# Kernel optimization log

Measured on AMD Instinct MI355X. Metric: run time of the kernel, lower is better.

Reference implementation:

```python
import jax, jax.numpy as jnp
import numpy as np

TOP_K = 3
TEMP = 5.0
EPS = 1e-12

def _normalize(x):
    # F.normalize(dim=-1): x / max(||x||_2, eps)
    n = jnp.linalg.norm(x, axis=-1, keepdims=True)
    return x / jnp.maximum(n, EPS)

def setup_inputs() -> dict:
    key = jax.random.key(0)
    ks = jax.random.split(key, 6)
    B, D, P = 32768, 512, 4096
    return {
        "regime_vector": jax.random.normal(ks[0], (B, D), dtype=jnp.float32),
        "prototypes": jax.random.normal(ks[1], (P, D), dtype=jnp.float32) * 0.1,
        "W1": jax.random.normal(ks[2], (32, 2 * D), dtype=jnp.float32) * 0.02,
        "b1": jax.random.normal(ks[3], (32,), dtype=jnp.float32) * 0.01,
        "W2": jax.random.normal(ks[4], (16, 32), dtype=jnp.float32) * 0.1,
        "b2": jax.random.normal(ks[5], (16,), dtype=jnp.float32) * 0.01,
    }

def reference(regime_vector, prototypes, W1, b1, W2, b2):
    # Cosine similarities: [B, P]
    sims = _normalize(regime_vector) @ _normalize(prototypes).T
    top_sims, top_idx = jax.lax.top_k(sims, TOP_K)          # [B, K]
    weights = jax.nn.softmax(top_sims * TEMP, axis=-1)       # [B, K]
    # Gather candidate prototypes: [B, K, D]
    cand = prototypes[top_idx]
    # Concat(regime, pattern) along feature dim: [B, K, 2D]
    B, K, D = cand.shape
    combined = jnp.concatenate(
        [jnp.broadcast_to(regime_vector[:, None, :], (B, K, D)), cand], axis=-1)
    # Two-layer MLP (torch Linear: x @ W.T + b)
    h = jax.nn.relu(jnp.einsum('bkd,hd->bkh', combined, W1) + b1)  # [B, K, 32]
    feats = jnp.einsum('bkh,oh->bko', h, W2) + b2                  # [B, K, 16]
    # Softmax-weighted sum over the K candidates
    pattern_features = jnp.einsum('bk,bko->bo', weights, feats)    # [B, 16]
    return pattern_features
```

## Files before the change

kernel.cpp:

```cpp
#include <hip/hip_runtime.h>
#include <stdint.h>


#define BDIM 512
#define NB   32768
#define NP   4096
#define PCH  256

typedef float  f32x4 __attribute__((ext_vector_type(4)));
typedef short  s16x8 __attribute__((ext_vector_type(8)));
typedef unsigned short u16;

typedef const __attribute__((address_space(1))) unsigned int* gas_t;
typedef __attribute__((address_space(3))) unsigned int* las_t;

__device__ __forceinline__ void gll16(const void* g, void* l) {
  __builtin_amdgcn_global_load_lds((gas_t)g, (las_t)l, 16, 0, 0);
}

__device__ __forceinline__ u16 f2bf(float f) {
  uint32_t u = __float_as_uint(f);
  return (u16)((u + 0x7FFFu + ((u >> 16) & 1u)) >> 16);
}
__device__ __forceinline__ uint32_t umx(uint32_t a, uint32_t b) { return a > b ? a : b; }
__device__ __forceinline__ uint32_t umn(uint32_t a, uint32_t b) { return a > b ? b : a; }

__device__ __forceinline__ uint32_t packkey(float v, int col) {
  uint32_t u = __float_as_uint(v);
  uint32_t mp = u ^ (uint32_t)(((int)u >> 31) | 0x80000000);
  return (mp & 0xFFFFF000u) | (uint32_t)col;
}
__device__ __forceinline__ float unpackf(uint32_t k) {
  uint32_t mbits = k & 0xFFFFF000u;
  uint32_t u = (mbits & 0x80000000u) ? (mbits ^ 0x80000000u) : ~mbits;
  return __uint_as_float(u);
}

__device__ __forceinline__ void bmerge(uint32_t* a, const uint32_t* b) {
  uint32_t t[8];
#pragma unroll
  for (int i = 0; i < 8; ++i) t[i] = umx(a[i], b[7 - i]);
#pragma unroll
  for (int i = 0; i < 4; ++i) { uint32_t x = umx(t[i], t[i + 4]), y = umn(t[i], t[i + 4]); t[i] = x; t[i + 4] = y; }
#pragma unroll
  for (int g = 0; g < 8; g += 4)
#pragma unroll
    for (int i = 0; i < 2; ++i) { uint32_t x = umx(t[g + i], t[g + i + 2]), y = umn(t[g + i], t[g + i + 2]); t[g + i] = x; t[g + i + 2] = y; }
#pragma unroll
  for (int p = 0; p < 8; p += 2) { uint32_t x = umx(t[p], t[p + 1]), y = umn(t[p], t[p + 1]); t[p] = x; t[p + 1] = y; }
#pragma unroll
  for (int i = 0; i < 8; ++i) a[i] = t[i];
}
__device__ __forceinline__ void mergeshfl(uint32_t* a, int mask) {
  uint32_t b[8];
#pragma unroll
  for (int i = 0; i < 8; ++i) b[i] = (uint32_t)__shfl_xor((int)a[i], mask, 64);
  bmerge(a, b);
}

__global__ __launch_bounds__(256) void prep_kernel(
    const float* __restrict__ src, const float* __restrict__ W1, int w1_off,
    int mode, u16* __restrict__ obf, float* __restrict__ onrm,
    float* __restrict__ oproj, float* __restrict__ onf32)
{
  __shared__ float rows[16][512];
  __shared__ float pscr[16][8][32];
  const int t = threadIdx.x, l = t & 63, w = t >> 6;
  const long rowbase = (long)blockIdx.x * 16;

  {
    const int r = t >> 4, c0 = (t & 15) * 32;
    const float4* gp = (const float4*)(src + (rowbase + r) * BDIM + c0);
    float4* dp = (float4*)&rows[r][c0];
#pragma unroll
    for (int i = 0; i < 8; ++i) dp[i] = gp[i];
  }
  float wreg[64];
  {
    const int h = t & 31, seg = t >> 5;
    const float* wp = W1 + h * 1024 + w1_off + seg * 64;
#pragma unroll
    for (int i = 0; i < 64; ++i) wreg[i] = wp[i];
  }
  __syncthreads();

#pragma unroll
  for (int i = 0; i < 4; ++i) {
    const int r = w * 4 + i;
    const long row = rowbase + r;
    float4 a = *(const float4*)&rows[r][4 * l];
    float4 c = *(const float4*)&rows[r][256 + 4 * l];
    float ss = a.x * a.x + a.y * a.y + a.z * a.z + a.w * a.w
             + c.x * c.x + c.y * c.y + c.z * c.z + c.w * c.w;
#pragma unroll
    for (int msk = 1; msk < 64; msk <<= 1) ss += __shfl_xor(ss, msk, 64);
    const float n = fmaxf(sqrtf(ss), 1e-12f);
    float4 qa, qc;
    qa.x = a.x / n; qa.y = a.y / n; qa.z = a.z / n; qa.w = a.w / n;
    qc.x = c.x / n; qc.y = c.y / n; qc.z = c.z / n; qc.w = c.w / n;
    ushort4 u0, u1;
    u0.x = f2bf(qa.x); u0.y = f2bf(qa.y); u0.z = f2bf(qa.z); u0.w = f2bf(qa.w);
    u1.x = f2bf(qc.x); u1.y = f2bf(qc.y); u1.z = f2bf(qc.z); u1.w = f2bf(qc.w);
    if (mode == 0) {
      if (l == 0) onrm[row] = n;
      *(ushort4*)(obf + row * BDIM + 4 * l) = u0;
      *(ushort4*)(obf + row * BDIM + 256 + 4 * l) = u1;
    } else {
      char* base = (char*)obf;
      *(ushort4*)(base + ((long)(l >> 4) * NP + row) * 128 + 8 * (l & 15)) = u0;
      *(ushort4*)(base + ((long)(4 + (l >> 4)) * NP + row) * 128 + 8 * (l & 15)) = u1;
      *(float4*)(onf32 + row * BDIM + 4 * l) = qa;
      *(float4*)(onf32 + row * BDIM + 256 + 4 * l) = qc;
    }
  }

  const int h = t & 31, seg = t >> 5;
  for (int r = 0; r < 16; ++r) {
    float p = 0.f;
#pragma unroll
    for (int j = 0; j < 16; ++j) {
      const float4 rv = *(const float4*)&rows[r][seg * 64 + 4 * j];
      p = fmaf(wreg[4 * j + 0], rv.x, p);
      p = fmaf(wreg[4 * j + 1], rv.y, p);
      p = fmaf(wreg[4 * j + 2], rv.z, p);
      p = fmaf(wreg[4 * j + 3], rv.w, p);
    }
    pscr[r][seg][h] = p;
  }
  __syncthreads();
#pragma unroll
  for (int q = 0; q < 2; ++q) {
    const int idx = t + q * 256;
    const int rr = idx >> 5, hh = idx & 31;
    float s = 0.f;
#pragma unroll
    for (int sg = 0; sg < 8; ++sg) s += pscr[rr][sg][hh];
    oproj[(rowbase + rr) * 32 + hh] = s;
  }
}

__global__ __launch_bounds__(256, 2) void topk_kernel(
    const u16* __restrict__ Rn,
    const u16* __restrict__ Pk,
    uint32_t* __restrict__ keys8)
{
  __shared__ uint4 lds4[5120];
  char* ldsb = (char*)lds4;

  const int t = threadIdx.x, l = t & 63, wid = t >> 6;
  const int wp = wid >> 1;
  const int wr = wid & 1;
  const int g = l >> 4, m = l & 15;
  const long rb = (long)blockIdx.x * 64;
  const char* Pkb = (const char*)Pk;
  const char* Rnb = (const char*)Rn;
  const int swsrc = 16 * ((l & 7) ^ ((l >> 3) & 7));
  const int lrow8 = (l >> 3);

  f32x4 acc[8][2];
  uint32_t k3[2][3];
  float thr[2];
#pragma unroll
  for (int fn = 0; fn < 2; ++fn) {
    thr[fn] = -1e30f;
#pragma unroll
    for (int i = 0; i < 3; ++i) k3[fn][i] = 0u;
  }

#define ISSUE(buf, ni_, kp_)                                                   \
  do {                                                                         \
    char* lp_ = ldsb + (buf) * 40960;                                          \
    const char* pg = Pkb + ((long)(kp_) * NP + (ni_) * PCH) * 128;             \
    _Pragma("unroll")                                                          \
    for (int i_ = 0; i_ < 8; ++i_) {                                           \
      const int ch_ = wid * 8 + i_;                                            \
      gll16(pg + ch_ * 1024 + lrow8 * 128 + swsrc, lp_ + ch_ * 1024);          \
    }                                                                          \
    _Pragma("unroll")                                                          \
    for (int j_ = 0; j_ < 2; ++j_) {                                           \
      const int ch_ = wid * 2 + j_;                                            \
      gll16(Rnb + (rb + ch_ * 8 + lrow8) * 1024 + (kp_) * 128 + swsrc,         \
            lp_ + 32768 + ch_ * 1024);                                         \
    }                                                                          \
  } while (0)

  ISSUE(0, 0, 0);

  for (int ni = 0; ni < 16; ++ni) {
#pragma unroll
    for (int fm = 0; fm < 8; ++fm)
#pragma unroll
      for (int fn = 0; fn < 2; ++fn) acc[fm][fn] = (f32x4){0.f, 0.f, 0.f, 0.f};

    for (int kp = 0; kp < 8; ++kp) {
      const int ph = ni * 8 + kp;
      asm volatile("s_waitcnt vmcnt(0)" ::: "memory");
      __builtin_amdgcn_s_barrier();
      const int nph = ph + 1;
      if (nph < 128) ISSUE(nph & 1, nph >> 3, nph & 7);
      __builtin_amdgcn_sched_barrier(0);
      const char* lp = ldsb + (ph & 1) * 40960;
      const char* lr = lp + 32768;
      const int sw = 16 * (m & 7);
#pragma unroll
      for (int ks = 0; ks < 2; ++ks) {
        const int koff = (ks * 64 + 16 * g) ^ sw;
        const char* pbr = lr + (wr * 32 + m) * 128 + koff;
        const char* pa = lp + (wp * 128 + m) * 128 + koff;
        uint4 b0 = *(const uint4*)(pbr);
        uint4 b1 = *(const uint4*)(pbr + 2048);
#pragma unroll
        for (int fm = 0; fm < 8; ++fm) {
          uint4 a4 = *(const uint4*)(pa + fm * 2048);
          acc[fm][0] = __builtin_amdgcn_mfma_f32_16x16x32_bf16(
              __builtin_bit_cast(s16x8, a4), __builtin_bit_cast(s16x8, b0),
              acc[fm][0], 0, 0, 0);
          acc[fm][1] = __builtin_amdgcn_mfma_f32_16x16x32_bf16(
              __builtin_bit_cast(s16x8, a4), __builtin_bit_cast(s16x8, b1),
              acc[fm][1], 0, 0, 0);
        }
      }
    }

    const int pb0 = ni * PCH + wp * 128 + 4 * g;
#pragma unroll
    for (int fn = 0; fn < 2; ++fn) {
#pragma unroll
      for (int fm = 0; fm < 8; ++fm) {
        const f32x4 v = acc[fm][fn];
        const float m4 = fmaxf(fmaxf(v[0], v[1]), fmaxf(v[2], v[3]));
        if (m4 > thr[fn]) {
#pragma unroll
          for (int r = 0; r < 4; ++r) {
            uint32_t kk = packkey(v[r], pb0 + fm * 16 + r);
            uint32_t mx0 = umx(k3[fn][0], kk), mn0 = umn(k3[fn][0], kk);
            k3[fn][0] = mx0; kk = mn0;
            uint32_t mx1 = umx(k3[fn][1], kk), mn1 = umn(k3[fn][1], kk);
            k3[fn][1] = mx1; kk = mn1;
            k3[fn][2] = umx(k3[fn][2], kk);
          }
          thr[fn] = unpackf(k3[fn][2]);
        }
      }
    }
  }
#undef ISSUE

  uint32_t* mrg = (uint32_t*)ldsb;
  uint32_t cur[2][8];
#pragma unroll
  for (int fn = 0; fn < 2; ++fn) {
    cur[fn][0] = k3[fn][0]; cur[fn][1] = k3[fn][1]; cur[fn][2] = k3[fn][2];
#pragma unroll
    for (int i = 3; i < 8; ++i) cur[fn][i] = 0u;
    mergeshfl(cur[fn], 16);
    mergeshfl(cur[fn], 32);
  }
  __syncthreads();
#pragma unroll
  for (int fn = 0; fn < 2; ++fn)
    if (wp == 1 && g == fn) {
      uint32_t* d = mrg + (wr * 32 + fn * 16 + m) * 8;
      uint4 a; a.x = cur[fn][0]; a.y = cur[fn][1]; a.z = cur[fn][2]; a.w = cur[fn][3];
      uint4 b; b.x = cur[fn][4]; b.y = cur[fn][5]; b.z = cur[fn][6]; b.w = cur[fn][7];
      *(uint4*)(d) = a; *(uint4*)(d + 4) = b;
    }
  __syncthreads();
#pragma unroll
  for (int fn = 0; fn < 2; ++fn)
    if (wp == 0 && g == fn) {
      const int row = wr * 32 + fn * 16 + m;
      uint32_t oth[8];
#pragma unroll
      for (int i = 0; i < 8; ++i) oth[i] = mrg[row * 8 + i];
      bmerge(cur[fn], oth);
      uint32_t* d = keys8 + (rb + row) * 8;
      uint4 a; a.x = cur[fn][0]; a.y = cur[fn][1]; a.z = cur[fn][2]; a.w = cur[fn][3];
      uint4 b; b.x = cur[fn][4]; b.y = cur[fn][5]; b.z = cur[fn][6]; b.w = cur[fn][7];
      *(uint4*)(d) = a; *(uint4*)(d + 4) = b;
    }
}

__global__ __launch_bounds__(256) void finalize_kernel(
    const float* __restrict__ regime, const float* __restrict__ protoNf,
    const uint32_t* __restrict__ keys8, const float* __restrict__ nrm_r,
    const float* __restrict__ rproj, const float* __restrict__ cproj,
    const float* __restrict__ b1, const float* __restrict__ W2,
    const float* __restrict__ b2, float* __restrict__ out)
{
  __shared__ float rlds[4][512];
  const int t = threadIdx.x, l = t & 63, w = t >> 6;
  const long b = (long)blockIdx.x * 4 + w;

  {
    const float n = nrm_r[b];
    const float4* gp = (const float4*)(regime + b * BDIM);
    float4 v0 = gp[l], v1 = gp[64 + l];
    v0.x /= n; v0.y /= n; v0.z /= n; v0.w /= n;
    v1.x /= n; v1.y /= n; v1.z /= n; v1.w /= n;
    *(float4*)&rlds[w][4 * l] = v0;
    *(float4*)&rlds[w][256 + 4 * l] = v1;
  }
  __syncthreads();

  const int j = l >> 3;
  const uint32_t key = keys8[b * 8 + j];
  const int pj = (int)(key & 0xFFFu);

  double dd = 0.0;
  {
    const float4* pp = (const float4*)(protoNf + (long)pj * BDIM);
    const float4* rr = (const float4*)&rlds[w][0];
#pragma unroll
    for (int u = 0; u < 16; ++u) {
      const float4 p4 = pp[(l & 7) + 8 * u];
      const float4 r4 = rr[(l & 7) + 8 * u];
      dd = fma((double)p4.x, (double)r4.x, dd);
      dd = fma((double)p4.y, (double)r4.y, dd);
      dd = fma((double)p4.z, (double)r4.z, dd);
      dd = fma((double)p4.w, (double)r4.w, dd);
    }
  }
  dd += __shfl_xor(dd, 1, 64);
  dd += __shfl_xor(dd, 2, 64);
  dd += __shfl_xor(dd, 4, 64);

  double sall[8]; int pall[8];
#pragma unroll
  for (int q = 0; q < 8; ++q) {
    sall[q] = __shfl(dd, q * 8, 64);
    pall[q] = __shfl(pj, q * 8, 64);
  }
  double vv[3]; int ppi[3]; unsigned chosen = 0;
#pragma unroll
  for (int r = 0; r < 3; ++r) {
    double bv = -1e301; int bp = 0x7FFFFFFF; int bq = 0;
#pragma unroll
    for (int q = 0; q < 8; ++q) {
      const bool ex = (chosen >> q) & 1u;
      const bool better = !ex && ((sall[q] > bv) || (sall[q] == bv && pall[q] < bp));
      bv = better ? sall[q] : bv;
      bp = better ? pall[q] : bp;
      bq = better ? q : bq;
    }
    vv[r] = bv; ppi[r] = bp; chosen |= 1u << bq;
  }
  const float v0f = (float)vv[0], v1f = (float)vv[1], v2f = (float)vv[2];
  const float e1 = expf(5.f * (v1f - v0f));
  const float e2 = expf(5.f * (v2f - v0f));
  const float winv = 1.f / (1.f + e1 + e2);
  const float w0 = winv, w1 = e1 * winv, w2 = e2 * winv;

  const int hu = l & 31, o = l & 15;
  const float rpv = rproj[b * 32 + hu];
  const float b1v = b1[hu];
  float w2row[32];
#pragma unroll
  for (int hh = 0; hh < 32; ++hh) w2row[hh] = W2[o * 32 + hh];
  float outacc = (l < 16) ? b2[o] : 0.f;
#pragma unroll
  for (int k = 0; k < 3; ++k) {
    const float cpv = cproj[(long)ppi[k] * 32 + hu];
    const float hval = fmaxf(rpv + cpv + b1v, 0.f);
    float f = 0.f;
#pragma unroll
    for (int hh = 0; hh < 32; ++hh) f = fmaf(w2row[hh], __shfl(hval, hh, 64), f);
    const float wk = (k == 0) ? w0 : ((k == 1) ? w1 : w2);
    outacc = fmaf(wk, f, outacc);
  }
  if (l < 16) out[b * 16 + o] = outacc;
}

extern "C" void kernel_launch(void* const* d_in, const int* in_sizes, int n_in,
                              void* d_out, int out_size, void* d_ws, size_t ws_size,
                              hipStream_t stream)
{
  (void)in_sizes; (void)n_in; (void)out_size; (void)ws_size;
  const float* regime = (const float*)d_in[0];
  const float* protos = (const float*)d_in[1];
  const float* W1     = (const float*)d_in[2];
  const float* b1     = (const float*)d_in[3];
  const float* W2     = (const float*)d_in[4];
  const float* b2     = (const float*)d_in[5];
  float* out = (float*)d_out;

  char* ws = (char*)d_ws;
  u16*      protoK  = (u16*)ws;      ws += (size_t)NP * BDIM * 2;
  u16*      regimeN = (u16*)ws;      ws += (size_t)NB * BDIM * 2;
  float*    protoNf = (float*)ws;    ws += (size_t)NP * BDIM * 4;
  float*    nrm_r   = (float*)ws;    ws += (size_t)NB * 4;
  float*    cproj   = (float*)ws;    ws += (size_t)NP * 32 * 4;
  float*    rproj   = (float*)ws;    ws += (size_t)NB * 32 * 4;
  uint32_t* keys8   = (uint32_t*)ws; ws += (size_t)NB * 8 * 4;

  hipLaunchKernelGGL(prep_kernel, dim3(NP / 16), dim3(256), 0, stream,
                     protos, W1, 512, 1, protoK, (float*)nullptr, cproj, protoNf);
  hipLaunchKernelGGL(prep_kernel, dim3(NB / 16), dim3(256), 0, stream,
                     regime, W1, 0, 0, regimeN, nrm_r, rproj, (float*)nullptr);
  hipLaunchKernelGGL(topk_kernel, dim3(512), dim3(256), 0, stream,
                     regimeN, protoK, keys8);
  hipLaunchKernelGGL(finalize_kernel, dim3(NB / 4), dim3(256), 0, stream,
                     regime, protoNf, keys8, nrm_r, rproj, cproj, b1, W2, b2, out);
}
```

Measured before the change: 425.6 us.

## Restructure top-k GEMM: 32x32 MFMA, register-streamed prototypes, LDS-resident regime rows

The similarity kernel is rebuilt. Each 512-thread block now loads 128 normalized regime rows into LDS once. Prototype fragments stream straight from global memory into registers with double buffering, replacing the per-phase LDS staging and barriers, and the 16x16x32 MFMA is swapped for 32x32x16. The prep kernel writes prototypes in a new fragment-ready layout to match. The cross-wave merge becomes an LDS gather followed by insertion into a top-8. Finalize now skips the fp64 rescoring dot product for candidates that clearly cannot reach the top 3. The cost is more registers per thread and a heavier load on global and L2 bandwidth for prototype reads. The approximate-score cutoff in finalize could change tie handling if the 4e-3 margin is too tight.

Result: slower. 573.4 us (+34.7%).

```diff
diff --git a/kernel.cpp b/kernel.cpp
--- a/kernel.cpp
+++ b/kernel.cpp
@@ -5,10 +5,10 @@
 #define BDIM 512
 #define NB   32768
 #define NP   4096
-#define PCH  256
-
-typedef float  f32x4 __attribute__((ext_vector_type(4)));
-typedef short  s16x8 __attribute__((ext_vector_type(8)));
+#define RPB  128
+
+typedef float  f32x16 __attribute__((ext_vector_type(16)));
+typedef short  s16x8  __attribute__((ext_vector_type(8)));
 typedef unsigned short u16;
 
 typedef const __attribute__((address_space(1))) unsigned int* gas_t;
@@ -34,6 +34,14 @@
   uint32_t mbits = k & 0xFFFFF000u;
   uint32_t u = (mbits & 0x80000000u) ? (mbits ^ 0x80000000u) : ~mbits;
   return __uint_as_float(u);
+}
+
+__device__ __forceinline__ void ins8(uint32_t* t, uint32_t k) {
+#pragma unroll
+  for (int i = 0; i < 8; ++i) {
+    uint32_t mx = umx(t[i], k), mn = umn(t[i], k);
+    t[i] = mx; k = mn;
+  }
 }
 
 __device__ __forceinline__ void bmerge(uint32_t* a, const uint32_t* b) {
@@ -95,22 +103,32 @@
 #pragma unroll
     for (int msk = 1; msk < 64; msk <<= 1) ss += __shfl_xor(ss, msk, 64);
     const float n = fmaxf(sqrtf(ss), 1e-12f);
-    float4 qa, qc;
-    qa.x = a.x / n; qa.y = a.y / n; qa.z = a.z / n; qa.w = a.w / n;
-    qc.x = c.x / n; qc.y = c.y / n; qc.z = c.z / n; qc.w = c.w / n;
-    ushort4 u0, u1;
-    u0.x = f2bf(qa.x); u0.y = f2bf(qa.y); u0.z = f2bf(qa.z); u0.w = f2bf(qa.w);
-    u1.x = f2bf(qc.x); u1.y = f2bf(qc.y); u1.z = f2bf(qc.z); u1.w = f2bf(qc.w);
     if (mode == 0) {
       if (l == 0) onrm[row] = n;
+      float4 qa, qc;
+      qa.x = a.x / n; qa.y = a.y / n; qa.z = a.z / n; qa.w = a.w / n;
+      qc.x = c.x / n; qc.y = c.y / n; qc.z = c.z / n; qc.w = c.w / n;
+      ushort4 u0, u1;
+      u0.x = f2bf(qa.x); u0.y = f2bf(qa.y); u0.z = f2bf(qa.z); u0.w = f2bf(qa.w);
+      u1.x = f2bf(qc.x); u1.y = f2bf(qc.y); u1.z = f2bf(qc.z); u1.w = f2bf(qc.w);
       *(ushort4*)(obf + row * BDIM + 4 * l) = u0;
       *(ushort4*)(obf + row * BDIM + 256 + 4 * l) = u1;
     } else {
-      char* base = (char*)obf;
-      *(ushort4*)(base + ((long)(l >> 4) * NP + row) * 128 + 8 * (l & 15)) = u0;
-      *(ushort4*)(base + ((long)(4 + (l >> 4)) * NP + row) * 128 + 8 * (l & 15)) = u1;
-      *(float4*)(onf32 + row * BDIM + 4 * l) = qa;
-      *(float4*)(onf32 + row * BDIM + 256 + 4 * l) = qc;
+      const float4 s0 = *(const float4*)&rows[r][8 * l];
+      const float4 s1 = *(const float4*)&rows[r][8 * l + 4];
+      float4 q0, q1;
+      q0.x = s0.x / n; q0.y = s0.y / n; q0.z = s0.z / n; q0.w = s0.w / n;
+      q1.x = s1.x / n; q1.y = s1.y / n; q1.z = s1.z / n; q1.w = s1.w / n;
+      ushort4 u0, u1;
+      u0.x = f2bf(q0.x); u0.y = f2bf(q0.y); u0.z = f2bf(q0.z); u0.w = f2bf(q0.w);
+      u1.x = f2bf(q1.x); u1.y = f2bf(q1.y); u1.z = f2bf(q1.z); u1.w = f2bf(q1.w);
+      const int rr = (int)row;
+      char* dst = (char*)obf + ((long)((rr >> 5) * 32 + (l >> 1)) * 1024)
+                + ((l & 1) * 32 + (rr & 31)) * 16;
+      *(ushort4*)(dst) = u0;
+      *(ushort4*)(dst + 8) = u1;
+      *(float4*)(onf32 + row * BDIM + 8 * l) = q0;
+      *(float4*)(onf32 + row * BDIM + 8 * l + 4) = q1;
     }
   }
 
@@ -139,25 +157,39 @@
   }
 }
 
-__global__ __launch_bounds__(256, 2) void topk_kernel(
+__global__ __launch_bounds__(512, 2) void topk_kernel(
     const u16* __restrict__ Rn,
     const u16* __restrict__ Pk,
     uint32_t* __restrict__ keys8)
 {
-  __shared__ uint4 lds4[5120];
+  __shared__ uint4 lds4[9216];
   char* ldsb = (char*)lds4;
+  uint32_t* mrg = (uint32_t*)(ldsb + 131072);
 
   const int t = threadIdx.x, l = t & 63, wid = t >> 6;
-  const int wp = wid >> 1;
-  const int wr = wid & 1;
-  const int g = l >> 4, m = l & 15;
-  const long rb = (long)blockIdx.x * 64;
-  const char* Pkb = (const char*)Pk;
-  const char* Rnb = (const char*)Rn;
-  const int swsrc = 16 * ((l & 7) ^ ((l >> 3) & 7));
-  const int lrow8 = (l >> 3);
-
-  f32x4 acc[8][2];
+  const int wp = wid & 3;
+  const int wn = wid >> 2;
+  const int l5 = l >> 5;
+  const long rb = (long)blockIdx.x * RPB;
+
+  for (int i = 0; i < 16; ++i) {
+    const int cell = i * 512 + t;
+    const int row = cell >> 6, c = cell & 63;
+    const int csrc = c ^ (row & 7);
+    gll16((const char*)Rn + (rb + row) * 1024 + csrc * 16, ldsb + cell * 16);
+  }
+  asm volatile("s_waitcnt vmcnt(0)" ::: "memory");
+  __syncthreads();
+
+  const int row0 = wn * 64 + (l & 31);
+  const int row1 = row0 + 32;
+  const char* bb0 = ldsb + row0 * 1024;
+  const char* bb1 = ldsb + row1 * 1024;
+  const int sz0 = row0 & 7, sz1 = row1 & 7;
+
+  const char* Abase = (const char*)Pk + (long)(wp * 4 * 32) * 1024 + l * 16;
+
+  f32x16 acc[4][2];
   uint32_t k3[2][3];
   float thr[2];
 #pragma unroll
@@ -166,73 +198,73 @@
 #pragma unroll
     for (int i = 0; i < 3; ++i) k3[fn][i] = 0u;
   }
-
-#define ISSUE(buf, ni_, kp_)                                                   \
+  uint4 A0[8], A1[8];
+
+#define LOADH(BUF, AOFF)                                                       \
   do {                                                                         \
-    char* lp_ = ldsb + (buf) * 40960;                                          \
-    const char* pg = Pkb + ((long)(kp_) * NP + (ni_) * PCH) * 128;             \
     _Pragma("unroll")                                                          \
-    for (int i_ = 0; i_ < 8; ++i_) {                                           \
-      const int ch_ = wid * 8 + i_;                                            \
-      gll16(pg + ch_ * 1024 + lrow8 * 128 + swsrc, lp_ + ch_ * 1024);          \
-    }                                                                          \
-    _Pragma("unroll")                                                          \
-    for (int j_ = 0; j_ < 2; ++j_) {                                           \
-      const int ch_ = wid * 2 + j_;                                            \
-      gll16(Rnb + (rb + ch_ * 8 + lrow8) * 1024 + (kp_) * 128 + swsrc,         \
-            lp_ + 32768 + ch_ * 1024);                                         \
+    for (int fm_ = 0; fm_ < 4; ++fm_) {                                        \
+      _Pragma("unroll")                                                        \
+      for (int q_ = 0; q_ < 2; ++q_)                                           \
+        BUF[fm_ * 2 + q_] =                                                    \
+            *(const uint4*)(Abase + (AOFF) + fm_ * 32768 + q_ * 1024);         \
     }                                                                          \
   } while (0)
 
-  ISSUE(0, 0, 0);
-
-  for (int ni = 0; ni < 16; ++ni) {
-#pragma unroll
-    for (int fm = 0; fm < 8; ++fm)
-#pragma unroll
-      for (int fn = 0; fn < 2; ++fn) acc[fm][fn] = (f32x4){0.f, 0.f, 0.f, 0.f};
+#define COMPH(BUF, KB0)                                                        \
+  do {                                                                         \
+    _Pragma("unroll")                                                          \
+    for (int q_ = 0; q_ < 2; ++q_) {                                           \
+      const int kb_ = (KB0) + q_;                                              \
+      const int g_ = kb_ * 2 + l5;                                             \
+      const uint4 b0_ = *(const uint4*)(bb0 + ((g_ ^ sz0) << 4));              \
+      const uint4 b1_ = *(const uint4*)(bb1 + ((g_ ^ sz1) << 4));              \
+      _Pragma("unroll")                                                        \
+      for (int fm_ = 0; fm_ < 4; ++fm_) {                                      \
+        acc[fm_][0] = __builtin_amdgcn_mfma_f32_32x32x16_bf16(                 \
+            __builtin_bit_cast(s16x8, BUF[fm_ * 2 + q_]),                      \
+            __builtin_bit_cast(s16x8, b0_), acc[fm_][0], 0, 0, 0);             \
+        acc[fm_][1] = __builtin_amdgcn_mfma_f32_32x32x16_bf16(                 \
+            __builtin_bit_cast(s16x8, BUF[fm_ * 2 + q_]),                      \
+            __builtin_bit_cast(s16x8, b1_), acc[fm_][1], 0, 0, 0);             \
+      }                                                                        \
+    }                                                                          \
+  } while (0)
+
+  long aoff = 0;
+  LOADH(A0, aoff);
+  for (int ni = 0; ni < 8; ++ni) {
+#pragma unroll
+    for (int fm = 0; fm < 4; ++fm)
+#pragma unroll
+      for (int fn = 0; fn < 2; ++fn)
+#pragma unroll
+        for (int r = 0; r < 16; ++r) acc[fm][fn][r] = 0.f;
 
     for (int kp = 0; kp < 8; ++kp) {
-      const int ph = ni * 8 + kp;
-      asm volatile("s_waitcnt vmcnt(0)" ::: "memory");
-      __builtin_amdgcn_s_barrier();
-      const int nph = ph + 1;
-      if (nph < 128) ISSUE(nph & 1, nph >> 3, nph & 7);
-      __builtin_amdgcn_sched_barrier(0);
-      const char* lp = ldsb + (ph & 1) * 40960;
-      const char* lr = lp + 32768;
-      const int sw = 16 * (m & 7);
-#pragma unroll
-      for (int ks = 0; ks < 2; ++ks) {
-        const int koff = (ks * 64 + 16 * g) ^ sw;
-        const char* pbr = lr + (wr * 32 + m) * 128 + koff;
-        const char* pa = lp + (wp * 128 + m) * 128 + koff;
-        uint4 b0 = *(const uint4*)(pbr);
-        uint4 b1 = *(const uint4*)(pbr + 2048);
-#pragma unroll
-        for (int fm = 0; fm < 8; ++fm) {
-          uint4 a4 = *(const uint4*)(pa + fm * 2048);
-          acc[fm][0] = __builtin_amdgcn_mfma_f32_16x16x32_bf16(
-              __builtin_bit_cast(s16x8, a4), __builtin_bit_cast(s16x8, b0),
-              acc[fm][0], 0, 0, 0);
-          acc[fm][1] = __builtin_amdgcn_mfma_f32_16x16x32_bf16(
-              __builtin_bit_cast(s16x8, a4), __builtin_bit_cast(s16x8, b1),
-              acc[fm][1], 0, 0, 0);
-        }
-      }
-    }
-
-    const int pb0 = ni * PCH + wp * 128 + 4 * g;
-#pragma unroll
-    for (int fn = 0; fn < 2; ++fn) {
-#pragma unroll
-      for (int fm = 0; fm < 8; ++fm) {
-        const f32x4 v = acc[fm][fn];
-        const float m4 = fmaxf(fmaxf(v[0], v[1]), fmaxf(v[2], v[3]));
-        if (m4 > thr[fn]) {
-#pragma unroll
-          for (int r = 0; r < 4; ++r) {
-            uint32_t kk = packkey(v[r], pb0 + fm * 16 + r);
+      LOADH(A1, aoff + 2048);
+      COMPH(A0, kp * 4);
+      const long nxt = (kp < 7) ? (aoff + 4096) : (aoff + 4096 + 491520);
+      LOADH(A0, nxt);
+      COMPH(A1, kp * 4 + 2);
+      aoff += 4096;
+    }
+    aoff += 491520;
+
+#pragma unroll
+    for (int fm = 0; fm < 4; ++fm) {
+      const int pb32 = (ni * 16 + wp * 4 + fm) * 32 + 4 * l5;
+#pragma unroll
+      for (int fn = 0; fn < 2; ++fn) {
+        const f32x16 v = acc[fm][fn];
+        float mx = fmaxf(fmaxf(fmaxf(v[0], v[1]), fmaxf(v[2], v[3])),
+                         fmaxf(fmaxf(v[4], v[5]), fmaxf(v[6], v[7])));
+        mx = fmaxf(mx, fmaxf(fmaxf(fmaxf(v[8], v[9]), fmaxf(v[10], v[11])),
+                             fmaxf(fmaxf(v[12], v[13]), fmaxf(v[14], v[15]))));
+        if (mx > thr[fn]) {
+#pragma unroll
+          for (int r = 0; r < 16; ++r) {
+            uint32_t kk = packkey(v[r], pb32 + (r & 3) + 8 * (r >> 2));
             uint32_t mx0 = umx(k3[fn][0], kk), mn0 = umn(k3[fn][0], kk);
             k3[fn][0] = mx0; kk = mn0;
             uint32_t mx1 = umx(k3[fn][1], kk), mn1 = umn(k3[fn][1], kk);
@@ -244,41 +276,39 @@
       }
     }
   }
-#undef ISSUE
-
-  uint32_t* mrg = (uint32_t*)ldsb;
-  uint32_t cur[2][8];
-#pragma unroll
-  for (int fn = 0; fn < 2; ++fn) {
-    cur[fn][0] = k3[fn][0]; cur[fn][1] = k3[fn][1]; cur[fn][2] = k3[fn][2];
-#pragma unroll
-    for (int i = 3; i < 8; ++i) cur[fn][i] = 0u;
-    mergeshfl(cur[fn], 16);
-    mergeshfl(cur[fn], 32);
+#undef LOADH
+#undef COMPH
+
+  uint32_t cur0[8], cur1[8];
+  cur0[0] = k3[0][0]; cur0[1] = k3[0][1]; cur0[2] = k3[0][2];
+  cur1[0] = k3[1][0]; cur1[1] = k3[1][1]; cur1[2] = k3[1][2];
+#pragma unroll
+  for (int i = 3; i < 8; ++i) { cur0[i] = 0u; cur1[i] = 0u; }
+  mergeshfl(cur0, 32);
+  mergeshfl(cur1, 32);
+  if (l < 32) {
+    uint32_t* d0 = mrg + ((wn * 64 + l) * 4 + wp) * 8;
+    uint32_t* d1 = mrg + ((wn * 64 + 32 + l) * 4 + wp) * 8;
+    uint4 a0; a0.x = cur0[0]; a0.y = cur0[1]; a0.z = cur0[2]; a0.w = cur0[3];
+    uint4 b0; b0.x = cur0[4]; b0.y = cur0[5]; b0.z = cur0[6]; b0.w = cur0[7];
+    uint4 a1; a1.x = cur1[0]; a1.y = cur1[1]; a1.z = cur1[2]; a1.w = cur1[3];
+    uint4 b1; b1.x = cur1[4]; b1.y = cur1[5]; b1.z = cur1[6]; b1.w = cur1[7];
+    *(uint4*)(d0) = a0; *(uint4*)(d0 + 4) = b0;
+    *(uint4*)(d1) = a1; *(uint4*)(d1 + 4) = b1;
   }
   __syncthreads();
-#pragma unroll
-  for (int fn = 0; fn < 2; ++fn)
-    if (wp == 1 && g == fn) {
-      uint32_t* d = mrg + (wr * 32 + fn * 16 + m) * 8;
-      uint4 a; a.x = cur[fn][0]; a.y = cur[fn][1]; a.z = cur[fn][2]; a.w = cur[fn][3];
-      uint4 b; b.x = cur[fn][4]; b.y = cur[fn][5]; b.z = cur[fn][6]; b.w = cur[fn][7];
-      *(uint4*)(d) = a; *(uint4*)(d + 4) = b;
-    }
-  __syncthreads();
-#pragma unroll
-  for (int fn = 0; fn < 2; ++fn)
-    if (wp == 0 && g == fn) {
-      const int row = wr * 32 + fn * 16 + m;
-      uint32_t oth[8];
-#pragma unroll
-      for (int i = 0; i < 8; ++i) oth[i] = mrg[row * 8 + i];
-      bmerge(cur[fn], oth);
-      uint32_t* d = keys8 + (rb + row) * 8;
-      uint4 a; a.x = cur[fn][0]; a.y = cur[fn][1]; a.z = cur[fn][2]; a.w = cur[fn][3];
-      uint4 b; b.x = cur[fn][4]; b.y = cur[fn][5]; b.z = cur[fn][6]; b.w = cur[fn][7];
-      *(uint4*)(d) = a; *(uint4*)(d + 4) = b;
-    }
+  if (t < RPB) {
+    const uint32_t* s = mrg + t * 32;
+    uint32_t best[8];
+#pragma unroll
+    for (int i = 0; i < 8; ++i) best[i] = s[i];
+#pragma unroll
+    for (int j = 8; j < 32; ++j) ins8(best, s[j]);
+    uint32_t* d = keys8 + (rb + t) * 8;
+    uint4 a; a.x = best[0]; a.y = best[1]; a.z = best[2]; a.w = best[3];
+    uint4 b; b.x = best[4]; b.y = best[5]; b.z = best[6]; b.w = best[7];
+    *(uint4*)(d) = a; *(uint4*)(d + 4) = b;
+  }
 }
 
 __global__ __launch_bounds__(256) void finalize_kernel(
@@ -306,9 +336,13 @@
   const int j = l >> 3;
   const uint32_t key = keys8[b * 8 + j];
   const int pj = (int)(key & 0xFFFu);
+  const float aval = unpackf(key);
+  const uint32_t key3 = (uint32_t)__shfl((int)key, 16, 64);
+  const float a3 = unpackf(key3);
+  const int act = (j < 3) || (aval >= a3 - 4e-3f);
 
   double dd = 0.0;
-  {
+  if (act) {
     const float4* pp = (const float4*)(protoNf + (long)pj * BDIM);
     const float4* rr = (const float4*)&rlds[w][0];
 #pragma unroll
@@ -328,7 +362,9 @@
   double sall[8]; int pall[8];
 #pragma unroll
   for (int q = 0; q < 8; ++q) {
-    sall[q] = __shfl(dd, q * 8, 64);
+    double sq = __shfl(dd, q * 8, 64);
+    int aq = __shfl(act, q * 8, 64);
+    sall[q] = aq ? sq : -1e300;
     pall[q] = __shfl(pj, q * 8, 64);
   }
   double vv[3]; int ppi[3]; unsigned chosen = 0;
@@ -397,7 +433,7 @@
                      protos, W1, 512, 1, protoK, (float*)nullptr, cproj, protoNf);
   hipLaunchKernelGGL(prep_kernel, dim3(NB / 16), dim3(256), 0, stream,
                      regime, W1, 0, 0, regimeN, nrm_r, rproj, (float*)nullptr);
-  hipLaunchKernelGGL(topk_kernel, dim3(512), dim3(256), 0, stream,
+  hipLaunchKernelGGL(topk_kernel, dim3(NB / RPB), dim3(512), 0, stream,
                      regimeN, protoK, keys8);
   hipLaunchKernelGGL(finalize_kernel, dim3(NB / 4), dim3(256), 0, stream,
                      regime, protoNf, keys8, nrm_r, rproj, cproj, b1, W2, b2, out);
```
